# Performance work log

Measured on AMD Instinct MI355X. Metric: run time of the kernel, lower is better.

The kernel has to match this reference:

```python
import jax, jax.numpy as jnp
import numpy as np

BST_DEPTH = 6
NB_SPLIT = 2**BST_DEPTH - 1          # 63 internal (split) nodes
NB_NODES = 2**(BST_DEPTH + 1) - 1    # 127 total nodes (heap layout)
SPLIT = np.arange(NB_SPLIT)
DESC_L = 2 * SPLIT + 1               # left children of split nodes
DESC_R = 2 * SPLIT + 2               # right children of split nodes


def setup_inputs() -> dict:
    key = jax.random.key(0)
    kx, ka = jax.random.split(key)
    x = jax.random.normal(kx, (131072, 512), dtype=jnp.float32)
    A = jax.random.uniform(ka, (NB_SPLIT, 512), dtype=jnp.float32)  # torch.rand init
    return {"x": x, "A": A}


def _compute_q(x, A):
    # XA[:, t] is the split score of internal node t; XA == XA[:, split_nodes]
    XA = x @ A.T                                         # [N, nb_split]
    q = jnp.ones((x.shape[0], NB_NODES), dtype=XA.dtype)  # [N, nb_nodes]
    # Seed children of each split node. NOTE: sequential semantics matter —
    # the right-child write reads q[:, SPLIT] AFTER the left-child write
    # (odd-indexed split nodes were just updated), matching torch in-place ops.
    q = q.at[:, DESC_L].set(jnp.minimum(q[:, SPLIT], XA))
    q = q.at[:, DESC_R].set(jnp.minimum(q[:, SPLIT], -XA))
    # Propagate the running min from parents down the tree, one sweep per level.
    for _ in range(BST_DEPTH):
        q = q.at[:, DESC_L].set(jnp.minimum(q[:, DESC_L], q[:, SPLIT]))
        q = q.at[:, DESC_R].set(jnp.minimum(q[:, DESC_R], q[:, SPLIT]))
    return q


def reference(x, A):
    q = _compute_q(x, A)
    z = jnp.clip(q, 0.0, 1.0)  # pruned=False: no QP pruning branch
    return z
```

## Files before the change

kernel.cpp:

```cpp
#include <hip/hip_runtime.h>
#include <hip/hip_bf16.h>
#include <cstdint>

#define KD 512
#define BM 128
#define NT 256
#define NSPLIT 63
#define NNODES 127

typedef __attribute__((ext_vector_type(8))) short bf16x8;
typedef __attribute__((ext_vector_type(4))) float f32x4;

#define MFMA_B16(a, b, c) __builtin_amdgcn_mfma_f32_16x16x32_bf16(a, b, c, 0, 0, 0)

__device__ __forceinline__ unsigned short f2bf(float f) {
    return __builtin_bit_cast(unsigned short, __float2bfloat16(f));
}
__device__ __forceinline__ float bf2f(unsigned short h) {
    return __builtin_bit_cast(float, (unsigned)h << 16);
}
__device__ __forceinline__ unsigned pack2(float f0, float f1) {
    return (unsigned)f2bf(f0) | ((unsigned)f2bf(f1) << 16);
}

__device__ __forceinline__ void cvt8(f32x4 a, f32x4 b, bf16x8& hi, bf16x8& lo) {
    const unsigned short h0 = f2bf(a[0]), h1 = f2bf(a[1]), h2 = f2bf(a[2]), h3 = f2bf(a[3]);
    const unsigned short h4 = f2bf(b[0]), h5 = f2bf(b[1]), h6 = f2bf(b[2]), h7 = f2bf(b[3]);
    uint4 H = make_uint4((unsigned)h0 | ((unsigned)h1 << 16), (unsigned)h2 | ((unsigned)h3 << 16),
                         (unsigned)h4 | ((unsigned)h5 << 16), (unsigned)h6 | ((unsigned)h7 << 16));
    uint4 L = make_uint4(pack2(a[0] - bf2f(h0), a[1] - bf2f(h1)),
                         pack2(a[2] - bf2f(h2), a[3] - bf2f(h3)),
                         pack2(b[0] - bf2f(h4), b[1] - bf2f(h5)),
                         pack2(b[2] - bf2f(h6), b[3] - bf2f(h7)));
    hi = __builtin_bit_cast(bf16x8, H);
    lo = __builtin_bit_cast(bf16x8, L);
}

__device__ __forceinline__ void gload_lds16(const float* g, void* l) {
    __builtin_amdgcn_global_load_lds(
        (const __attribute__((address_space(1))) unsigned int*)g,
        (__attribute__((address_space(3))) unsigned int*)l, 16, 0, 0);
}

template<int T>
__device__ __forceinline__ void tree_walk(float qt, const float* __restrict__ srow,
                                          float* __restrict__ zrow, int part) {
    const float s  = srow[T];
    const float ql = fminf(qt, s);
    const float qr = fminf(qt, -s);
    if (((2 * T + 1) >> 5) == part) zrow[2 * T + 1] = fminf(fmaxf(ql, 0.f), 1.f);
    if (((2 * T + 2) >> 5) == part) zrow[2 * T + 2] = fminf(fmaxf(qr, 0.f), 1.f);
    if constexpr (2 * T + 1 < NSPLIT) tree_walk<2 * T + 1>(ql, srow, zrow, part);
    if constexpr (2 * T + 2 < NSPLIT) tree_walk<2 * T + 2>(qr, srow, zrow, part);
}

__global__ __launch_bounds__(NT, 2)
void lt_mfma4(const float* __restrict__ x, const float* __restrict__ A,
              float* __restrict__ out) {
    __shared__ __align__(16) unsigned char lds[65536];
    unsigned char* xb0 = lds;
    unsigned char* xb1 = lds + 16384;
    unsigned short* bhp = (unsigned short*)(lds + 32768);
    unsigned short* blp = (unsigned short*)(lds + 49152);

    const int tid  = threadIdx.x;
    const int wave = tid >> 6;
    const int lane = tid & 63;
    const int fr   = lane & 15;
    const int kb   = (lane >> 4) * 8;
    const int r0   = blockIdx.x * BM;
    const int m0   = wave * 32;

    const float* xg = x + (size_t)r0 * KD;
    const int brow = tid >> 2;
    const int bc   = tid & 3;
    const float* ag = A + (size_t)brow * KD + bc * 32;

    f32x4 acc[2][4];
#pragma unroll
    for (int i = 0; i < 2; ++i)
#pragma unroll
        for (int j = 0; j < 4; ++j) acc[i][j] = (f32x4)(0.f);

#pragma unroll
    for (int j = 0; j < 4; ++j) {
        const int u = j * 256 + tid;
        const int row = u >> 3;
        const int sp = (u & 7) ^ (row & 7);
        gload_lds16(xg + row * KD + sp * 4, xb0 + (size_t)u * 16);
    }

    const int m = fr & 7;
    const int u00 = (m0 + fr) * 8 + ((kb >> 2) ^ m);
    const int bo  = fr * 128 + 0;

#pragma unroll
    for (int q = 0; q < 4; ++q) {
#pragma unroll
        for (int p = 0; p < 4; ++p) {
            f32x4 a = (f32x4)(0.f), b = (f32x4)(0.f);
            if (brow < NSPLIT) {
                a = *reinterpret_cast<const f32x4*>(ag + q * 128 + p * 8);
                b = *reinterpret_cast<const f32x4*>(ag + q * 128 + p * 8 + 4);
            }
            bf16x8 hi, lo;
            cvt8(a, b, hi, lo);
            const int sl = (bc * 4 + p) ^ (brow & 7);
            *reinterpret_cast<bf16x8*>(bhp + brow * 128 + sl * 8) = hi;
            *reinterpret_cast<bf16x8*>(blp + brow * 128 + sl * 8) = lo;
        }
        __syncthreads();

#pragma unroll
        for (int tl = 0; tl < 4; ++tl) {
            const int t = q * 4 + tl;
            if (t + 1 < 16) {
                unsigned char* nb = ((t + 1) & 1) ? xb1 : xb0;
                const float* xgt = xg + (t + 1) * 32;
#pragma unroll
                for (int j = 0; j < 4; ++j) {
                    const int u = j * 256 + tid;
                    const int row = u >> 3;
                    const int sp = (u & 7) ^ (row & 7);
                    gload_lds16(xgt + row * KD + sp * 4, nb + (size_t)u * 16);
                }
            }
            const float* xbf = (const float*)((t & 1) ? xb1 : xb0);
            f32x4 va0 = *reinterpret_cast<const f32x4*>(xbf + u00 * 4);
            f32x4 vb0 = *reinterpret_cast<const f32x4*>(xbf + (u00 ^ 1) * 4);
            f32x4 va1 = *reinterpret_cast<const f32x4*>(xbf + (u00 + 128) * 4);
            f32x4 vb1 = *reinterpret_cast<const f32x4*>(xbf + ((u00 + 128) ^ 1) * 4);
            bf16x8 ah0, al0, ah1, al1;
            cvt8(va0, vb0, ah0, al0);
            cvt8(va1, vb1, ah1, al1);

            const int sb = (tl * 4 + (kb >> 3)) ^ m;
            const int bof = fr * 128 + sb * 8;
            bf16x8 bv0 = *reinterpret_cast<const bf16x8*>(bhp + bof);
            bf16x8 bv1 = *reinterpret_cast<const bf16x8*>(bhp + bof + 2048);
            bf16x8 bv2 = *reinterpret_cast<const bf16x8*>(bhp + bof + 4096);
            bf16x8 bv3 = *reinterpret_cast<const bf16x8*>(bhp + bof + 6144);

            acc[0][0] = MFMA_B16(ah0, bv0, acc[0][0]);
            acc[1][0] = MFMA_B16(ah1, bv0, acc[1][0]);
            acc[0][1] = MFMA_B16(ah0, bv1, acc[0][1]);
            acc[1][1] = MFMA_B16(ah1, bv1, acc[1][1]);
            acc[0][2] = MFMA_B16(ah0, bv2, acc[0][2]);
            acc[1][2] = MFMA_B16(ah1, bv2, acc[1][2]);
            acc[0][3] = MFMA_B16(ah0, bv3, acc[0][3]);
            acc[1][3] = MFMA_B16(ah1, bv3, acc[1][3]);
            acc[0][0] = MFMA_B16(al0, bv0, acc[0][0]);
            acc[1][0] = MFMA_B16(al1, bv0, acc[1][0]);
            acc[0][1] = MFMA_B16(al0, bv1, acc[0][1]);
            acc[1][1] = MFMA_B16(al1, bv1, acc[1][1]);
            acc[0][2] = MFMA_B16(al0, bv2, acc[0][2]);
            acc[1][2] = MFMA_B16(al1, bv2, acc[1][2]);
            acc[0][3] = MFMA_B16(al0, bv3, acc[0][3]);
            acc[1][3] = MFMA_B16(al1, bv3, acc[1][3]);
            bv0 = *reinterpret_cast<const bf16x8*>(blp + bof);
            bv1 = *reinterpret_cast<const bf16x8*>(blp + bof + 2048);
            bv2 = *reinterpret_cast<const bf16x8*>(blp + bof + 4096);
            bv3 = *reinterpret_cast<const bf16x8*>(blp + bof + 6144);
            acc[0][0] = MFMA_B16(ah0, bv0, acc[0][0]);
            acc[1][0] = MFMA_B16(ah1, bv0, acc[1][0]);
            acc[0][1] = MFMA_B16(ah0, bv1, acc[0][1]);
            acc[1][1] = MFMA_B16(ah1, bv1, acc[1][1]);
            acc[0][2] = MFMA_B16(ah0, bv2, acc[0][2]);
            acc[1][2] = MFMA_B16(ah1, bv2, acc[1][2]);
            acc[0][3] = MFMA_B16(ah0, bv3, acc[0][3]);
            acc[1][3] = MFMA_B16(ah1, bv3, acc[1][3]);

            __syncthreads();
        }
    }

    float* warea = (float*)(lds + 32768 + wave * 4160);
    float* zw    = (float*)(lds + wave * 8128);
    const int drow = (lane >> 4) * 4;
    const int trow = lane >> 2;
    const int part = lane & 3;

#pragma unroll
    for (int ph = 0; ph < 2; ++ph) {
#pragma unroll
        for (int nf = 0; nf < 4; ++nf)
#pragma unroll
            for (int rg = 0; rg < 4; ++rg)
                warea[(drow + rg) * 65 + nf * 16 + fr] = acc[ph][nf][rg];
        const float* srowp = warea + trow * 65;
        float* zrow = zw + trow * NNODES;
        if (part == 0) zrow[0] = 1.f;
        tree_walk<0>(1.f, srowp, zrow, part);

        float* og = out + (size_t)(r0 + m0 + ph * 16) * NNODES;
#pragma unroll
        for (int j = 0; j < 8; ++j) {
            const int idx = j * 64 + lane;
            if (idx < 508)
                *reinterpret_cast<f32x4*>(og + idx * 4) =
                    *reinterpret_cast<const f32x4*>((const float*)zw + idx * 4);
        }
    }
    (void)bo;
}

extern "C" void kernel_launch(void* const* d_in, const int* in_sizes, int n_in,
                              void* d_out, int out_size, void* d_ws, size_t ws_size,
                              hipStream_t stream) {
    const float* x = (const float*)d_in[0];
    const float* A = (const float*)d_in[1];
    float* out = (float*)d_out;
    const int nrows = in_sizes[0] / KD;
    const int grid = nrows / BM;
    lt_mfma4<<<dim3(grid), dim3(NT), 0, stream>>>(x, A, out);
}
```

Before: 89.02 us.

## Give each wave a private triple-buffered x pipeline and drop per-tile block barriers

Each wave now loads its own 32 rows of x into a private 3-slot LDS ring with global_load_lds, prefetching two tiles ahead and waiting with explicit vmcnt counts. Block-wide barriers happen only when a new quarter of A is staged into shared memory, not after every K tile. The aim is to remove the per-tile __syncthreads stalls and give the loads more time to land while the MFMAs run. In exchange LDS per block grows to 80 KB, which may cut occupancy below the two blocks per CU that the launch bounds request, and the hand-written waitcnt and sched_barrier timing is fragile.

```diff
diff --git a/kernel.cpp b/kernel.cpp
--- a/kernel.cpp
+++ b/kernel.cpp
@@ -7,23 +7,26 @@
 #define NT 256
 #define NSPLIT 63
 #define NNODES 127
+#define XWB 12288
+#define BH_OFF 49152
+#define BL_OFF 65536
 
 typedef __attribute__((ext_vector_type(8))) short bf16x8;
 typedef __attribute__((ext_vector_type(4))) float f32x4;
 
 #define MFMA_B16(a, b, c) __builtin_amdgcn_mfma_f32_16x16x32_bf16(a, b, c, 0, 0, 0)
 
-__device__ __forceinline__ unsigned short f2bf(float f) {
+static __device__ __forceinline__ unsigned short f2bf(float f) {
     return __builtin_bit_cast(unsigned short, __float2bfloat16(f));
 }
-__device__ __forceinline__ float bf2f(unsigned short h) {
+static __device__ __forceinline__ float bf2f(unsigned short h) {
     return __builtin_bit_cast(float, (unsigned)h << 16);
 }
-__device__ __forceinline__ unsigned pack2(float f0, float f1) {
+static __device__ __forceinline__ unsigned pack2(float f0, float f1) {
     return (unsigned)f2bf(f0) | ((unsigned)f2bf(f1) << 16);
 }
 
-__device__ __forceinline__ void cvt8(f32x4 a, f32x4 b, bf16x8& hi, bf16x8& lo) {
+static __device__ __forceinline__ void cvt8(f32x4 a, f32x4 b, bf16x8& hi, bf16x8& lo) {
     const unsigned short h0 = f2bf(a[0]), h1 = f2bf(a[1]), h2 = f2bf(a[2]), h3 = f2bf(a[3]);
     const unsigned short h4 = f2bf(b[0]), h5 = f2bf(b[1]), h6 = f2bf(b[2]), h7 = f2bf(b[3]);
     uint4 H = make_uint4((unsigned)h0 | ((unsigned)h1 << 16), (unsigned)h2 | ((unsigned)h3 << 16),
@@ -36,15 +39,21 @@
     lo = __builtin_bit_cast(bf16x8, L);
 }
 
-__device__ __forceinline__ void gload_lds16(const float* g, void* l) {
+static __device__ __forceinline__ void gload_lds16(const float* g, void* l) {
     __builtin_amdgcn_global_load_lds(
         (const __attribute__((address_space(1))) unsigned int*)g,
         (__attribute__((address_space(3))) unsigned int*)l, 16, 0, 0);
 }
 
+template<int N> static __device__ __forceinline__ void vmwait() {
+    if constexpr (N == 8)      asm volatile("s_waitcnt vmcnt(8)" ::: "memory");
+    else if constexpr (N == 4) asm volatile("s_waitcnt vmcnt(4)" ::: "memory");
+    else                       asm volatile("s_waitcnt vmcnt(0)" ::: "memory");
+}
+
 template<int T>
-__device__ __forceinline__ void tree_walk(float qt, const float* __restrict__ srow,
-                                          float* __restrict__ zrow, int part) {
+static __device__ __forceinline__ void tree_walk(float qt, const float* __restrict__ srow,
+                                                 float* __restrict__ zrow, int part) {
     const float s  = srow[T];
     const float ql = fminf(qt, s);
     const float qr = fminf(qt, -s);
@@ -54,27 +63,121 @@
     if constexpr (2 * T + 2 < NSPLIT) tree_walk<2 * T + 2>(qr, srow, zrow, part);
 }
 
+template<int Q>
+static __device__ __forceinline__ void stage_B(const float* ag, bool bvalid,
+                                               unsigned short* bhp, unsigned short* blp,
+                                               int brow, int slb) {
+#pragma unroll
+    for (int p = 0; p < 4; ++p) {
+        f32x4 a = (f32x4)(0.f), b = (f32x4)(0.f);
+        if (bvalid) {
+            a = *reinterpret_cast<const f32x4*>(ag + Q * 128 + p * 8);
+            b = *reinterpret_cast<const f32x4*>(ag + Q * 128 + p * 8 + 4);
+        }
+        bf16x8 hi, lo;
+        cvt8(a, b, hi, lo);
+        const int sl = (slb + p) ^ (brow & 7);
+        *reinterpret_cast<bf16x8*>(bhp + brow * 128 + sl * 8) = hi;
+        *reinterpret_cast<bf16x8*>(blp + brow * 128 + sl * 8) = lo;
+    }
+}
+
+template<int T>
+static __device__ __forceinline__ void tiles(
+        const float* xsrc, unsigned char* xw,
+        unsigned short* bhp, unsigned short* blp,
+        const float* ag, bool bvalid, int brow, int slb,
+        int fr, int kb, int m, f32x4 (&acc)[2][4]) {
+    if constexpr (T > 0 && (T & 3) == 0) {
+        __builtin_amdgcn_s_barrier();
+        stage_B<T / 4>(ag, bvalid, bhp, blp, brow, slb);
+        asm volatile("s_waitcnt lgkmcnt(0)" ::: "memory");
+        __builtin_amdgcn_s_barrier();
+    }
+    __builtin_amdgcn_sched_barrier(0);
+    if constexpr (T + 2 < 16) {
+        constexpr int wb = (T + 2) % 3;
+#pragma unroll
+        for (int j = 0; j < 4; ++j)
+            gload_lds16(xsrc + (T + 2) * 32 + j * 8 * KD, xw + wb * 4096 + j * 1024);
+    }
+    vmwait<(T <= 13 ? 8 : (T == 14 ? 4 : 0))>();
+    __builtin_amdgcn_sched_barrier(0);
+
+    constexpr int rb = T % 3;
+    const float* xbf = reinterpret_cast<const float*>(xw + rb * 4096);
+    f32x4 va0 = *reinterpret_cast<const f32x4*>(xbf + fr * 32 + kb);
+    f32x4 vb0 = *reinterpret_cast<const f32x4*>(xbf + fr * 32 + kb + 4);
+    f32x4 va1 = *reinterpret_cast<const f32x4*>(xbf + (16 + fr) * 32 + kb);
+    f32x4 vb1 = *reinterpret_cast<const f32x4*>(xbf + (16 + fr) * 32 + kb + 4);
+    bf16x8 ah0, al0, ah1, al1;
+    cvt8(va0, vb0, ah0, al0);
+    cvt8(va1, vb1, ah1, al1);
+
+    constexpr int tl = T & 3;
+    const int sb  = (tl * 4 + (kb >> 3)) ^ m;
+    const int bof = fr * 128 + sb * 8;
+    bf16x8 bv0 = *reinterpret_cast<const bf16x8*>(bhp + bof);
+    bf16x8 bv1 = *reinterpret_cast<const bf16x8*>(bhp + bof + 2048);
+    bf16x8 bv2 = *reinterpret_cast<const bf16x8*>(bhp + bof + 4096);
+    bf16x8 bv3 = *reinterpret_cast<const bf16x8*>(bhp + bof + 6144);
+
+    acc[0][0] = MFMA_B16(ah0, bv0, acc[0][0]);
+    acc[1][0] = MFMA_B16(ah1, bv0, acc[1][0]);
+    acc[0][1] = MFMA_B16(ah0, bv1, acc[0][1]);
+    acc[1][1] = MFMA_B16(ah1, bv1, acc[1][1]);
+    acc[0][2] = MFMA_B16(ah0, bv2, acc[0][2]);
+    acc[1][2] = MFMA_B16(ah1, bv2, acc[1][2]);
+    acc[0][3] = MFMA_B16(ah0, bv3, acc[0][3]);
+    acc[1][3] = MFMA_B16(ah1, bv3, acc[1][3]);
+    acc[0][0] = MFMA_B16(al0, bv0, acc[0][0]);
+    acc[1][0] = MFMA_B16(al1, bv0, acc[1][0]);
+    acc[0][1] = MFMA_B16(al0, bv1, acc[0][1]);
+    acc[1][1] = MFMA_B16(al1, bv1, acc[1][1]);
+    acc[0][2] = MFMA_B16(al0, bv2, acc[0][2]);
+    acc[1][2] = MFMA_B16(al1, bv2, acc[1][2]);
+    acc[0][3] = MFMA_B16(al0, bv3, acc[0][3]);
+    acc[1][3] = MFMA_B16(al1, bv3, acc[1][3]);
+    bv0 = *reinterpret_cast<const bf16x8*>(blp + bof);
+    bv1 = *reinterpret_cast<const bf16x8*>(blp + bof + 2048);
+    bv2 = *reinterpret_cast<const bf16x8*>(blp + bof + 4096);
+    bv3 = *reinterpret_cast<const bf16x8*>(blp + bof + 6144);
+    acc[0][0] = MFMA_B16(ah0, bv0, acc[0][0]);
+    acc[1][0] = MFMA_B16(ah1, bv0, acc[1][0]);
+    acc[0][1] = MFMA_B16(ah0, bv1, acc[0][1]);
+    acc[1][1] = MFMA_B16(ah1, bv1, acc[1][1]);
+    acc[0][2] = MFMA_B16(ah0, bv2, acc[0][2]);
+    acc[1][2] = MFMA_B16(ah1, bv2, acc[1][2]);
+    acc[0][3] = MFMA_B16(ah0, bv3, acc[0][3]);
+    acc[1][3] = MFMA_B16(ah1, bv3, acc[1][3]);
+
+    if constexpr (T + 1 < 16)
+        tiles<T + 1>(xsrc, xw, bhp, blp, ag, bvalid, brow, slb, fr, kb, m, acc);
+}
+
 __global__ __launch_bounds__(NT, 2)
-void lt_mfma4(const float* __restrict__ x, const float* __restrict__ A,
+void lt_mfma5(const float* __restrict__ x, const float* __restrict__ A,
               float* __restrict__ out) {
-    __shared__ __align__(16) unsigned char lds[65536];
-    unsigned char* xb0 = lds;
-    unsigned char* xb1 = lds + 16384;
-    unsigned short* bhp = (unsigned short*)(lds + 32768);
-    unsigned short* blp = (unsigned short*)(lds + 49152);
+    __shared__ __align__(16) unsigned char lds[81920];
+    unsigned short* bhp = (unsigned short*)(lds + BH_OFF);
+    unsigned short* blp = (unsigned short*)(lds + BL_OFF);
 
     const int tid  = threadIdx.x;
     const int wave = tid >> 6;
     const int lane = tid & 63;
     const int fr   = lane & 15;
     const int kb   = (lane >> 4) * 8;
+    const int m    = fr & 7;
     const int r0   = blockIdx.x * BM;
     const int m0   = wave * 32;
 
-    const float* xg = x + (size_t)r0 * KD;
+    unsigned char* xw = lds + wave * XWB;
+    const float* xsrc = x + (size_t)(r0 + m0 + (lane >> 3)) * KD + (lane & 7) * 4;
+
     const int brow = tid >> 2;
-    const int bc   = tid & 3;
-    const float* ag = A + (size_t)brow * KD + bc * 32;
+    const int slb  = (tid & 3) * 4;
+    const bool bvalid = brow < NSPLIT;
+    const float* ag = A + (size_t)brow * KD + (tid & 3) * 32;
 
     f32x4 acc[2][4];
 #pragma unroll
@@ -83,99 +186,21 @@
         for (int j = 0; j < 4; ++j) acc[i][j] = (f32x4)(0.f);
 
 #pragma unroll
-    for (int j = 0; j < 4; ++j) {
-        const int u = j * 256 + tid;
-        const int row = u >> 3;
-        const int sp = (u & 7) ^ (row & 7);
-        gload_lds16(xg + row * KD + sp * 4, xb0 + (size_t)u * 16);
-    }
-
-    const int m = fr & 7;
-    const int u00 = (m0 + fr) * 8 + ((kb >> 2) ^ m);
-    const int bo  = fr * 128 + 0;
-
-#pragma unroll
-    for (int q = 0; q < 4; ++q) {
-#pragma unroll
-        for (int p = 0; p < 4; ++p) {
-            f32x4 a = (f32x4)(0.f), b = (f32x4)(0.f);
-            if (brow < NSPLIT) {
-                a = *reinterpret_cast<const f32x4*>(ag + q * 128 + p * 8);
-                b = *reinterpret_cast<const f32x4*>(ag + q * 128 + p * 8 + 4);
-            }
-            bf16x8 hi, lo;
-            cvt8(a, b, hi, lo);
-            const int sl = (bc * 4 + p) ^ (brow & 7);
-            *reinterpret_cast<bf16x8*>(bhp + brow * 128 + sl * 8) = hi;
-            *reinterpret_cast<bf16x8*>(blp + brow * 128 + sl * 8) = lo;
-        }
-        __syncthreads();
-
-#pragma unroll
-        for (int tl = 0; tl < 4; ++tl) {
-            const int t = q * 4 + tl;
-            if (t + 1 < 16) {
-                unsigned char* nb = ((t + 1) & 1) ? xb1 : xb0;
-                const float* xgt = xg + (t + 1) * 32;
-#pragma unroll
-                for (int j = 0; j < 4; ++j) {
-                    const int u = j * 256 + tid;
-                    const int row = u >> 3;
-                    const int sp = (u & 7) ^ (row & 7);
-                    gload_lds16(xgt + row * KD + sp * 4, nb + (size_t)u * 16);
-                }
-            }
-            const float* xbf = (const float*)((t & 1) ? xb1 : xb0);
-            f32x4 va0 = *reinterpret_cast<const f32x4*>(xbf + u00 * 4);
-            f32x4 vb0 = *reinterpret_cast<const f32x4*>(xbf + (u00 ^ 1) * 4);
-            f32x4 va1 = *reinterpret_cast<const f32x4*>(xbf + (u00 + 128) * 4);
-            f32x4 vb1 = *reinterpret_cast<const f32x4*>(xbf + ((u00 + 128) ^ 1) * 4);
-            bf16x8 ah0, al0, ah1, al1;
-            cvt8(va0, vb0, ah0, al0);
-            cvt8(va1, vb1, ah1, al1);
-
-            const int sb = (tl * 4 + (kb >> 3)) ^ m;
-            const int bof = fr * 128 + sb * 8;
-            bf16x8 bv0 = *reinterpret_cast<const bf16x8*>(bhp + bof);
-            bf16x8 bv1 = *reinterpret_cast<const bf16x8*>(bhp + bof + 2048);
-            bf16x8 bv2 = *reinterpret_cast<const bf16x8*>(bhp + bof + 4096);
-            bf16x8 bv3 = *reinterpret_cast<const bf16x8*>(bhp + bof + 6144);
-
-            acc[0][0] = MFMA_B16(ah0, bv0, acc[0][0]);
-            acc[1][0] = MFMA_B16(ah1, bv0, acc[1][0]);
-            acc[0][1] = MFMA_B16(ah0, bv1, acc[0][1]);
-            acc[1][1] = MFMA_B16(ah1, bv1, acc[1][1]);
-            acc[0][2] = MFMA_B16(ah0, bv2, acc[0][2]);
-            acc[1][2] = MFMA_B16(ah1, bv2, acc[1][2]);
-            acc[0][3] = MFMA_B16(ah0, bv3, acc[0][3]);
-            acc[1][3] = MFMA_B16(ah1, bv3, acc[1][3]);
-            acc[0][0] = MFMA_B16(al0, bv0, acc[0][0]);
-            acc[1][0] = MFMA_B16(al1, bv0, acc[1][0]);
-            acc[0][1] = MFMA_B16(al0, bv1, acc[0][1]);
-            acc[1][1] = MFMA_B16(al1, bv1, acc[1][1]);
-            acc[0][2] = MFMA_B16(al0, bv2, acc[0][2]);
-            acc[1][2] = MFMA_B16(al1, bv2, acc[1][2]);
-            acc[0][3] = MFMA_B16(al0, bv3, acc[0][3]);
-            acc[1][3] = MFMA_B16(al1, bv3, acc[1][3]);
-            bv0 = *reinterpret_cast<const bf16x8*>(blp + bof);
-            bv1 = *reinterpret_cast<const bf16x8*>(blp + bof + 2048);
-            bv2 = *reinterpret_cast<const bf16x8*>(blp + bof + 4096);
-            bv3 = *reinterpret_cast<const bf16x8*>(blp + bof + 6144);
-            acc[0][0] = MFMA_B16(ah0, bv0, acc[0][0]);
-            acc[1][0] = MFMA_B16(ah1, bv0, acc[1][0]);
-            acc[0][1] = MFMA_B16(ah0, bv1, acc[0][1]);
-            acc[1][1] = MFMA_B16(ah1, bv1, acc[1][1]);
-            acc[0][2] = MFMA_B16(ah0, bv2, acc[0][2]);
-            acc[1][2] = MFMA_B16(ah1, bv2, acc[1][2]);
-            acc[0][3] = MFMA_B16(ah0, bv3, acc[0][3]);
-            acc[1][3] = MFMA_B16(ah1, bv3, acc[1][3]);
-
-            __syncthreads();
-        }
-    }
-
-    float* warea = (float*)(lds + 32768 + wave * 4160);
-    float* zw    = (float*)(lds + wave * 8128);
+    for (int j = 0; j < 4; ++j)
+        gload_lds16(xsrc + j * 8 * KD, xw + j * 1024);
+#pragma unroll
+    for (int j = 0; j < 4; ++j)
+        gload_lds16(xsrc + 32 + j * 8 * KD, xw + 4096 + j * 1024);
+    stage_B<0>(ag, bvalid, bhp, blp, brow, slb);
+    asm volatile("s_waitcnt lgkmcnt(0)" ::: "memory");
+    __builtin_amdgcn_s_barrier();
+
+    tiles<0>(xsrc, xw, bhp, blp, ag, bvalid, brow, slb, fr, kb, m, acc);
+
+    __syncthreads();
+
+    float* warea = (float*)(lds + BH_OFF + wave * 4160);
+    float* zw    = (float*)(lds + wave * XWB);
     const int drow = (lane >> 4) * 4;
     const int trow = lane >> 2;
     const int part = lane & 3;
@@ -201,7 +226,6 @@
                     *reinterpret_cast<const f32x4*>((const float*)zw + idx * 4);
         }
     }
-    (void)bo;
 }
 
 extern "C" void kernel_launch(void* const* d_in, const int* in_sizes, int n_in,
@@ -212,5 +236,5 @@
     float* out = (float*)d_out;
     const int nrows = in_sizes[0] / KD;
     const int grid = nrows / BM;
-    lt_mfma4<<<dim3(grid), dim3(NT), 0, stream>>>(x, A, out);
-}
+    lt_mfma5<<<dim3(grid), dim3(NT), 0, stream>>>(x, A, out);
+}
```

New measurement: 88.33 us. Within noise of the previous version (-0.8%).
